# Kernel optimization log

Hardware: AMD Instinct MI355X
Metric: run time of the kernel (lower is better)

Reference implementation:

```python
import jax, jax.numpy as jnp
import numpy as np


def setup_inputs() -> dict:
    key = jax.random.key(0)
    k1, k2 = jax.random.split(key)
    B, H, Lq, Lk, D = 4, 8, 2048, 2048, 64
    input1 = jax.random.normal(k1, (B, H, Lq, D), dtype=jnp.float32)   # query [B,H,Lq,d]
    input2 = jax.random.normal(k2, (B, H, D, Lk), dtype=jnp.float32)   # key   [B,H,d,Lk]
    return {"input1": input1, "input2": input2}


def reference(input1, input2):
    # out[b,h,i,j] = sum_c (q[b,h,i,c] - k[b,h,c,j])**2
    # Expanded: ||q_i||^2 + ||k_j||^2 - 2 q_i . k_j  (avoids [B,H,Lq,Lk,d] blowup)
    q2 = jnp.sum(input1 * input1, axis=-1)[..., :, None]   # [B,H,Lq,1]
    k2 = jnp.sum(input2 * input2, axis=-2)[..., None, :]   # [B,H,1,Lk]
    qk = jnp.einsum("bhid,bhdj->bhij", input1, input2)     # [B,H,Lq,Lk]
    return q2 + k2 - 2.0 * qk
```

## Files before the change

### kernel.cpp

```cpp
#include <hip/hip_runtime.h>
#include <hip/hip_bf16.h>


#define BH 32
#define LQ 2048
#define LK 2048
#define DD 64
#define TM 128
#define TN 128
#define LDT 72
#define SST 136

typedef __attribute__((ext_vector_type(8))) short short8;
typedef __attribute__((ext_vector_type(4))) float f32x4;

__device__ __forceinline__ unsigned f2bf(float f) {
  unsigned u = __builtin_bit_cast(unsigned, f);
  u += 0x7fffu + ((u >> 16) & 1u);
  return u >> 16;
}
__device__ __forceinline__ float bflo(unsigned w) { return __builtin_bit_cast(float, w << 16); }
__device__ __forceinline__ float bfhi(unsigned w) { return __builtin_bit_cast(float, w & 0xffff0000u); }

__global__ __launch_bounds__(256, 4) void sg_kernel(const float* __restrict__ Q,
                                                    const float* __restrict__ K,
                                                    float* __restrict__ out) {
  __shared__ __align__(16) unsigned short smem[2 * TM * LDT];
  __shared__ float norms[256];

  unsigned short* As = smem;
  unsigned short* Bt = smem + TM * LDT;

  const int bh  = blockIdx.z;
  const int gm0 = blockIdx.y * TM;
  const int gn0 = blockIdx.x * TN;
  const int tid = threadIdx.x;

  {
    const float* qbase = Q + ((size_t)bh * LQ + gm0) * DD;
#pragma unroll
    for (int it = 0; it < 4; ++it) {
      int c = it * 256 + tid;
      const float4* p = (const float4*)(qbase + c * 8);
      float4 a = p[0];
      float4 b = p[1];
      int4 pk;
      pk.x = (int)(f2bf(a.x) | (f2bf(a.y) << 16));
      pk.y = (int)(f2bf(a.z) | (f2bf(a.w) << 16));
      pk.z = (int)(f2bf(b.x) | (f2bf(b.y) << 16));
      pk.w = (int)(f2bf(b.z) | (f2bf(b.w) << 16));
      *(int4*)&As[(c >> 3) * LDT + (c & 7) * 8] = pk;
    }
  }

  {
    int col = tid & 127;
    int c0b = (tid >> 7) * 32;
    const float* kp = K + (size_t)bh * DD * LK + gn0 + col;
#pragma unroll
    for (int it = 0; it < 8; ++it) {
      int c0 = c0b + it * 4;
      float v0 = kp[(size_t)(c0 + 0) * LK];
      float v1 = kp[(size_t)(c0 + 1) * LK];
      float v2 = kp[(size_t)(c0 + 2) * LK];
      float v3 = kp[(size_t)(c0 + 3) * LK];
      uint2 w;
      w.x = f2bf(v0) | (f2bf(v1) << 16);
      w.y = f2bf(v2) | (f2bf(v3) << 16);
      *(uint2*)&Bt[col * LDT + c0] = w;
    }
  }

  __syncthreads();

  {
    float s = 0.f;
#pragma unroll
    for (int ch = 0; ch < 8; ++ch) {
      int4 pk = *(const int4*)&smem[tid * LDT + ch * 8];
      float v;
      v = bflo((unsigned)pk.x); s += v * v; v = bfhi((unsigned)pk.x); s += v * v;
      v = bflo((unsigned)pk.y); s += v * v; v = bfhi((unsigned)pk.y); s += v * v;
      v = bflo((unsigned)pk.z); s += v * v; v = bfhi((unsigned)pk.z); s += v * v;
      v = bflo((unsigned)pk.w); s += v * v; v = bfhi((unsigned)pk.w); s += v * v;
    }
    norms[tid] = s;
  }

  const int wave = tid >> 6;
  const int lane = tid & 63;
  const int wm   = (wave >> 1) * 64;
  const int wn   = (wave & 1) * 64;
  const int n15  = lane & 15;
  const int qd   = lane >> 4;

  f32x4 acc[4][4];
#pragma unroll
  for (int mi = 0; mi < 4; ++mi)
#pragma unroll
    for (int ni = 0; ni < 4; ++ni)
      acc[mi][ni] = (f32x4){0.f, 0.f, 0.f, 0.f};

#pragma unroll
  for (int kk = 0; kk < DD; kk += 32) {
    short8 a[4], b[4];
#pragma unroll
    for (int mi = 0; mi < 4; ++mi)
      a[mi] = *(const short8*)&As[(wm + mi * 16 + n15) * LDT + kk + qd * 8];
#pragma unroll
    for (int ni = 0; ni < 4; ++ni)
      b[ni] = *(const short8*)&Bt[(wn + ni * 16 + n15) * LDT + kk + qd * 8];
#pragma unroll
    for (int mi = 0; mi < 4; ++mi)
#pragma unroll
      for (int ni = 0; ni < 4; ++ni)
        acc[mi][ni] = __builtin_amdgcn_mfma_f32_16x16x32_bf16(a[mi], b[ni], acc[mi][ni], 0, 0, 0);
  }

  float* sf = (float*)smem;
  const size_t obase = ((size_t)bh * LQ + gm0) * (size_t)LK + gn0;

  for (int h = 0; h < 2; ++h) {
    __syncthreads();
    if ((wave >> 1) == h) {
#pragma unroll
      for (int mi = 0; mi < 4; ++mi) {
#pragma unroll
        for (int ni = 0; ni < 4; ++ni) {
          float k2v = norms[128 + wn + ni * 16 + n15];
#pragma unroll
          for (int r = 0; r < 4; ++r) {
            int lr = mi * 16 + qd * 4 + r;
            sf[lr * SST + wn + ni * 16 + n15] =
                norms[h * 64 + lr] + k2v - 2.0f * acc[mi][ni][r];
          }
        }
      }
    }
    __syncthreads();
    int rr = tid >> 5;
    int cc = (tid & 31) * 4;
#pragma unroll
    for (int it = 0; it < 8; ++it) {
      int row = it * 8 + rr;
      float4 v = *(const float4*)&sf[row * SST + cc];
      *(float4*)&out[obase + (size_t)(h * 64 + row) * LK + cc] = v;
    }
  }
}

extern "C" void kernel_launch(void* const* d_in, const int* in_sizes, int n_in,
                              void* d_out, int out_size, void* d_ws, size_t ws_size,
                              hipStream_t stream) {
  const float* Q = (const float*)d_in[0];
  const float* K = (const float*)d_in[1];
  float* out = (float*)d_out;
  dim3 grid(LK / TN, LQ / TM, BH);
  sg_kernel<<<grid, 256, 0, stream>>>(Q, K, out);
}
```

Measured before the change: 564.6 us.

## Compute norms in fp32 from global loads and store MFMA results directly

```diff
diff --git a/kernel.cpp b/kernel.cpp
--- a/kernel.cpp
+++ b/kernel.cpp
@@ -9,7 +9,6 @@
 #define TM 128
 #define TN 128
 #define LDT 72
-#define SST 136
 
 typedef __attribute__((ext_vector_type(8))) short short8;
 typedef __attribute__((ext_vector_type(4))) float f32x4;
@@ -19,14 +18,12 @@
   u += 0x7fffu + ((u >> 16) & 1u);
   return u >> 16;
 }
-__device__ __forceinline__ float bflo(unsigned w) { return __builtin_bit_cast(float, w << 16); }
-__device__ __forceinline__ float bfhi(unsigned w) { return __builtin_bit_cast(float, w & 0xffff0000u); }
 
 __global__ __launch_bounds__(256, 4) void sg_kernel(const float* __restrict__ Q,
                                                     const float* __restrict__ K,
                                                     float* __restrict__ out) {
   __shared__ __align__(16) unsigned short smem[2 * TM * LDT];
-  __shared__ float norms[256];
+  __shared__ __align__(16) float norms[256];
 
   unsigned short* As = smem;
   unsigned short* Bt = smem + TM * LDT;
@@ -36,6 +33,9 @@
   const int gn0 = blockIdx.x * TN;
   const int tid = threadIdx.x;
 
+  norms[tid] = 0.f;
+  __syncthreads();
+
   {
     const float* qbase = Q + ((size_t)bh * LQ + gm0) * DD;
 #pragma unroll
@@ -44,6 +44,9 @@
       const float4* p = (const float4*)(qbase + c * 8);
       float4 a = p[0];
       float4 b = p[1];
+      float s = a.x * a.x + a.y * a.y + a.z * a.z + a.w * a.w +
+                b.x * b.x + b.y * b.y + b.z * b.z + b.w * b.w;
+      atomicAdd(&norms[c >> 3], s);
       int4 pk;
       pk.x = (int)(f2bf(a.x) | (f2bf(a.y) << 16));
       pk.y = (int)(f2bf(a.z) | (f2bf(a.w) << 16));
@@ -57,6 +60,7 @@
     int col = tid & 127;
     int c0b = (tid >> 7) * 32;
     const float* kp = K + (size_t)bh * DD * LK + gn0 + col;
+    float s = 0.f;
 #pragma unroll
     for (int it = 0; it < 8; ++it) {
       int c0 = c0b + it * 4;
@@ -64,28 +68,16 @@
       float v1 = kp[(size_t)(c0 + 1) * LK];
       float v2 = kp[(size_t)(c0 + 2) * LK];
       float v3 = kp[(size_t)(c0 + 3) * LK];
+      s += v0 * v0 + v1 * v1 + v2 * v2 + v3 * v3;
       uint2 w;
       w.x = f2bf(v0) | (f2bf(v1) << 16);
       w.y = f2bf(v2) | (f2bf(v3) << 16);
       *(uint2*)&Bt[col * LDT + c0] = w;
     }
+    atomicAdd(&norms[128 + col], s);
   }
 
   __syncthreads();
-
-  {
-    float s = 0.f;
-#pragma unroll
-    for (int ch = 0; ch < 8; ++ch) {
-      int4 pk = *(const int4*)&smem[tid * LDT + ch * 8];
-      float v;
-      v = bflo((unsigned)pk.x); s += v * v; v = bfhi((unsigned)pk.x); s += v * v;
-      v = bflo((unsigned)pk.y); s += v * v; v = bfhi((unsigned)pk.y); s += v * v;
-      v = bflo((unsigned)pk.z); s += v * v; v = bfhi((unsigned)pk.z); s += v * v;
-      v = bflo((unsigned)pk.w); s += v * v; v = bfhi((unsigned)pk.w); s += v * v;
-    }
-    norms[tid] = s;
-  }
 
   const int wave = tid >> 6;
   const int lane = tid & 63;
@@ -117,34 +109,25 @@
         acc[mi][ni] = __builtin_amdgcn_mfma_f32_16x16x32_bf16(a[mi], b[ni], acc[mi][ni], 0, 0, 0);
   }
 
-  float* sf = (float*)smem;
-  const size_t obase = ((size_t)bh * LQ + gm0) * (size_t)LK + gn0;
+  f32x4 q2v[4];
+  float k2s[4];
+#pragma unroll
+  for (int mi = 0; mi < 4; ++mi)
+    q2v[mi] = *(const f32x4*)&norms[wm + mi * 16 + qd * 4];
+#pragma unroll
+  for (int ni = 0; ni < 4; ++ni)
+    k2s[ni] = norms[128 + wn + ni * 16 + n15];
 
-  for (int h = 0; h < 2; ++h) {
-    __syncthreads();
-    if ((wave >> 1) == h) {
+  float* pob = out + ((size_t)bh * LQ + gm0 + wm + qd * 4) * (size_t)LK + gn0 + wn + n15;
 #pragma unroll
-      for (int mi = 0; mi < 4; ++mi) {
+  for (int mi = 0; mi < 4; ++mi) {
 #pragma unroll
-        for (int ni = 0; ni < 4; ++ni) {
-          float k2v = norms[128 + wn + ni * 16 + n15];
+    for (int r = 0; r < 4; ++r) {
+      float* pr = pob + (size_t)(mi * 16 + r) * LK;
+      float q2 = q2v[mi][r];
 #pragma unroll
-          for (int r = 0; r < 4; ++r) {
-            int lr = mi * 16 + qd * 4 + r;
-            sf[lr * SST + wn + ni * 16 + n15] =
-                norms[h * 64 + lr] + k2v - 2.0f * acc[mi][ni][r];
-          }
-        }
-      }
-    }
-    __syncthreads();
-    int rr = tid >> 5;
-    int cc = (tid & 31) * 4;
-#pragma unroll
-    for (int it = 0; it < 8; ++it) {
-      int row = it * 8 + rr;
-      float4 v = *(const float4*)&sf[row * SST + cc];
-      *(float4*)&out[obase + (size_t)(h * 64 + row) * LK + cc] = v;
+      for (int ni = 0; ni < 4; ++ni)
+        pr[ni * 16] = fmaf(-2.0f, acc[mi][ni][r], q2 + k2s[ni]);
     }
   }
 }
```

Result: slower. 616.9 us (+9.3%).
